# Kernel tuning notes

Hardware: AMD Instinct MI355X
Metric: run time of the kernel (lower is better)

The kernel has to match this reference:

```python
import jax, jax.numpy as jnp
import numpy as np
from jax import lax

SHIFT = 32  # shift_range from init
EPS_NORM = 1e-12
EPS_MASK = 1e-6


def _l2_normalize_flat(x):
    # F.normalize(x.reshape(B,-1)): per-sample L2 normalize with eps 1e-12
    B = x.shape[0]
    flat = x.reshape(B, -1)
    n = jnp.linalg.norm(flat, axis=1, keepdims=True)
    return (flat / jnp.maximum(n, EPS_NORM)).reshape(x.shape)


def setup_inputs() -> dict:
    key = jax.random.key(0)
    k1, k2 = jax.random.split(key)
    grd_feature = jax.random.normal(k1, (8, 32, 32, 32), dtype=jnp.float32)
    sat_feature = jax.random.normal(k2, (8, 32, 128, 128), dtype=jnp.float32)
    return {"grd_feature": grd_feature, "sat_feature": sat_feature, "test_method": 1}


def reference(grd_feature, sat_feature, test_method):
    # test_method == 1 path (default); test_method in {0,1} only differ in divisor
    M, C, H_s, W_s = sat_feature.shape
    N, _, H, W = grd_feature.shape
    kH = min(H, H_s - 2 * SHIFT)
    kW = min(W, W_s - 2 * SHIFT)

    # center-crop ground template to (kH, kW) and L2-normalize per sample
    gh0, gw0 = H // 2 - kH // 2, W // 2 - kW // 2
    grd = grd_feature[:, :, gh0:gh0 + 2 * (kH // 2), gw0:gw0 + 2 * (kW // 2)]
    N_, _, H_k, W_k = grd.shape
    grd = _l2_normalize_flat(grd)

    # center-crop satellite to search region and L2-normalize per sample
    sh0 = H_s // 2 - SHIFT - kH // 2
    sw0 = W_s // 2 - SHIFT - kW // 2
    sat = sat_feature[:, :, sh0:sh0 + 2 * (SHIFT + kH // 2), sw0:sw0 + 2 * (SHIFT + kW // 2)]
    _, _, H_i, W_i = sat.shape
    sat = _l2_normalize_flat(sat)

    # all-pairs cross-correlation: corr[m, n, y, x] (torch grouped-conv on repeated sat
    # is equivalent to a plain VALID conv of sat with all N ground filters)
    corr = lax.conv_general_dilated(
        sat, grd, window_strides=(1, 1), padding='VALID',
        dimension_numbers=('NCHW', 'OIHW', 'NCHW'))  # [M, N, Ho, Wo]
    Ho, Wo = corr.shape[2], corr.shape[3]

    # sliding-window sum of |sat|^2 (avg_pool with divisor_override=1, summed over C)
    s2 = jnp.sum(sat * sat, axis=1)  # [M, H_i, W_i]
    partical = lax.reduce_window(s2, jnp.float32(0), lax.add,
                                 (1, H_k, W_k), (1, 1, 1), 'VALID')  # [M, Ho, Wo]
    if test_method == 0:
        denom = jnp.sqrt(partical)
    else:
        denom = partical
    corr = corr / jnp.maximum(denom[:, None], EPS_NORM)

    similarity_matrix = jnp.max(corr, axis=(2, 3))  # [M, N]

    # diagonal pairs (m == n): peak localization
    diag = jnp.diagonal(corr, axis1=0, axis2=1)        # [Ho, Wo, M]
    diag = jnp.transpose(diag, (2, 0, 1)).reshape(M, -1)
    max_index = jnp.argmax(diag, axis=-1)
    pos_h = max_index // Wo
    pos_w = max_index % Wo

    grd_mask = (jnp.abs(jnp.sum(grd, axis=1)) > EPS_MASK).astype(jnp.float32)  # [N, H_k, W_k]

    def place(ph, pw, gm):
        z = jnp.zeros((1, H_i, W_i), dtype=jnp.float32)
        return lax.dynamic_update_slice(z, gm[None], (0, ph, pw))

    mask = jax.vmap(place)(pos_h, pos_w, grd_mask)  # [M, 1, H_i, W_i]
    return similarity_matrix, mask
```

## Files before the change

kernel.cpp:

```cpp
#include <hip/hip_runtime.h>
#include <stdint.h>

typedef unsigned short u16;
typedef unsigned int u32;
typedef unsigned long long u64;
typedef __bf16 bf16x8 __attribute__((ext_vector_type(8)));
typedef float floatx4 __attribute__((ext_vector_type(4)));

#define DEVI static __device__ __forceinline__

DEVI u16 f2bf(float f) {
  uint32_t u = __builtin_bit_cast(uint32_t, f);
  u += 0x7FFFu + ((u >> 16) & 1u);
  return (u16)(u >> 16);
}
DEVI float bf2f(u16 b) { return __builtin_bit_cast(float, (uint32_t)b << 16); }

DEVI u32 encf(float f) {
  u32 u = __builtin_bit_cast(u32, f);
  return (u >> 31) ? ~u : (u | 0x80000000u);
}
DEVI float decf(u32 e) {
  u32 u = (e >> 31) ? (e & 0x7FFFFFFFu) : ~e;
  return __builtin_bit_cast(float, u);
}

static constexpr size_t OFF_CORRP = 0;
static constexpr size_t OFF_SATT  = OFF_CORRP + (size_t)4*270400*4;
static constexpr size_t OFF_GRDP  = OFF_SATT + (size_t)8*4*96*96*8*2;
static constexpr size_t OFF_S2    = OFF_GRDP + (size_t)4*1024*16*8*2;
static constexpr size_t OFF_PART  = OFF_S2   + (size_t)73728*4;
static constexpr size_t OFF_NRMP  = OFF_PART + (size_t)33800*4;
static constexpr size_t OFF_GNRM  = OFF_NRMP + 768*4;
static constexpr size_t OFF_MASK  = OFF_GNRM + 32;
static constexpr size_t OFF_PMAX  = OFF_MASK + (size_t)8192*4;
static constexpr size_t OFF_CNT   = OFF_PMAX + 320*4;
static constexpr size_t OFF_CAND  = OFF_CNT  + 512;

__global__ __launch_bounds__(256) void k_prep(
    const float* __restrict__ grd, const float* __restrict__ sat,
    u16* __restrict__ sTh, u16* __restrict__ gP,
    float* __restrict__ s2, float* __restrict__ nrmp,
    float* __restrict__ gnrm, float* __restrict__ gmask,
    u32* __restrict__ cnts) {
  __shared__ float L[32*100];
  __shared__ float red[256];
  const int t = threadIdx.x;
  if (blockIdx.x < 768) {
    const int m = blockIdx.x / 96, y = blockIdx.x - (blockIdx.x / 96) * 96;
    #pragma unroll
    for (int k = 0; k < 3; ++k) {
      const int idx = k*256 + t;
      const int c = idx / 24, xq = idx - c*24;
      const float4 v = *(const float4*)(sat + (((size_t)m*32 + c)*128 + (16+y))*128 + 16 + xq*4);
      *(float4*)(&L[c*100 + xq*4]) = v;
    }
    __syncthreads();
    float ss = 0.f;
    if (t < 96) {
      #pragma unroll
      for (int c = 0; c < 32; ++c) { const float v = L[c*100 + t]; ss += v*v; }
      s2[(size_t)m*9216 + y*96 + t] = ss;
    }
    red[t] = ss; __syncthreads();
    for (int s = 128; s > 0; s >>= 1) { if (t < s) red[t] += red[t+s]; __syncthreads(); }
    if (t == 0) nrmp[m*96 + y] = red[0];
    for (int idx = t; idx < 384; idx += 256) {
      const int cb = idx / 96, x = idx - cb*96;
      union { u16 us[8]; uint4 v4; } P;
      #pragma unroll
      for (int e = 0; e < 8; ++e) P.us[e] = f2bf(L[(cb*8+e)*100 + x]);
      *(uint4*)(&sTh[(((size_t)m*4+cb)*9216 + (size_t)y*96 + x)*8]) = P.v4;
    }
  } else if (blockIdx.x == 776) {
    if (t < 72) cnts[t] = 0u;
  } else {
    const int n = blockIdx.x - 768;
    float nn = 0.f, scs[4];
    #pragma unroll
    for (int it = 0; it < 4; ++it) {
      const int pidx = it*256 + t;
      float vals[32]; float sc = 0.f;
      #pragma unroll
      for (int c = 0; c < 32; ++c) {
        const float v = grd[((size_t)n*32 + c)*1024 + pidx];
        vals[c] = v; sc += v; nn += v*v;
      }
      scs[it] = sc;
      #pragma unroll
      for (int cb = 0; cb < 4; ++cb) {
        union { u16 us[8]; uint4 v4; } ph, pl;
        #pragma unroll
        for (int e = 0; e < 8; ++e) {
          const float v = vals[cb*8+e];
          const u16 h = f2bf(v); ph.us[e] = h; pl.us[e] = f2bf(v - bf2f(h));
        }
        const size_t o = ((size_t)cb*1024 + pidx)*128;
        *(uint4*)(&gP[o + (size_t)n*8])     = ph.v4;
        *(uint4*)(&gP[o + (size_t)(n+8)*8]) = pl.v4;
      }
    }
    red[t] = nn; __syncthreads();
    for (int s = 128; s > 0; s >>= 1) { if (t < s) red[t] += red[t+s]; __syncthreads(); }
    const float gn = fmaxf(sqrtf(red[0]), 1e-12f);
    if (t == 0) gnrm[n] = red[0];
    const float thr = 1e-6f * gn;
    #pragma unroll
    for (int it = 0; it < 4; ++it)
      gmask[n*1024 + it*256 + t] = (fabsf(scs[it]) > thr) ? 1.f : 0.f;
  }
}

__global__ __launch_bounds__(256, 4) void k_conv(
    const u16* __restrict__ satT, const u16* __restrict__ gP,
    const float* __restrict__ s2, float* __restrict__ corr_p,
    float* __restrict__ part)
{
  __shared__ __align__(16) u16 patch[36*48*8];

  const int bi = blockIdx.x;
  const int tid = threadIdx.x;

  if (bi >= 1824) {
    float* S  = (float*)patch;
    float* HS = S + 40*96;
    const int pb = bi - 1824;
    const int pm = pb / 9, ysl = (pb - pm*9)*8;
    const int nrows = (65 - ysl) < 8 ? (65 - ysl) : 8;
    const int scnt  = (96 - ysl) < 40 ? (96 - ysl) : 40;
    for (int idx = tid; idx < scnt*96; idx += 256)
      S[idx] = s2[(size_t)pm*9216 + (size_t)ysl*96 + idx];
    __syncthreads();
    const int hrows = nrows + 31;
    for (int idx = tid; idx < hrows*65; idx += 256) {
      const int r = idx / 65, xo = idx - r*65;
      const float* p = &S[r*96 + xo];
      float s = 0.f;
      #pragma unroll
      for (int j = 0; j < 32; ++j) s += p[j];
      HS[idx] = s;
    }
    __syncthreads();
    for (int idx = tid; idx < nrows*65; idx += 256) {
      const int r = idx / 65, xo = idx - r*65;
      float s = 0.f;
      #pragma unroll
      for (int i = 0; i < 32; ++i) s += HS[(r+i)*65 + xo];
      part[(size_t)pm*4225 + (size_t)(ysl+r)*65 + xo] = s;
    }
    return;
  }

  const int wave = tid >> 6, lane = tid & 63;
  const int pr = lane & 15, q = lane >> 4;

  if (bi >= 1664) {
    const int e = bi - 1664;
    const int cb = e & 3;
    const int yt = (e >> 2) % 5;
    const int m  = e / 20;
    const int ybase = yt * 13;
    const size_t rowbase = ((size_t)(m*4 + cb) * 96 + ybase) * 96;
    for (int k = tid; k < 44*32; k += 256) {
      const int rho = k >> 5, px = k & 31;
      *(uint4*)(&patch[(size_t)k*8]) =
          *(const uint4*)(&satT[(rowbase + (size_t)rho*96 + 64 + px)*8]);
    }
    __syncthreads();
    const int prc = pr < 13 ? pr : 12;
    floatx4 acc = (floatx4){0.f, 0.f, 0.f, 0.f};
    #pragma unroll
    for (int jbi = 0; jbi < 2; ++jbi) {
      const int jb = wave*2 + jbi;
      const int px_e = jb*4 + q;
      const u16* bp = gP + ((size_t)cb*1024 + (size_t)(jb*4+q))*128 + (size_t)pr*8;
      uint4 Br[8];
      #pragma unroll
      for (int ii = 0; ii < 8; ++ii) Br[ii] = *(const uint4*)(bp + (size_t)ii*4096);
      uint4 Ah[8];
      #pragma unroll
      for (int s = 0; s < 6; ++s)
        Ah[s] = *(const uint4*)(&patch[((size_t)(prc + s)*32 + px_e)*8]);
      #pragma unroll
      for (int i = 0; i < 32; ++i) {
        if (i < 26)
          Ah[(i+6)&7] = *(const uint4*)(&patch[((size_t)(prc + i + 6)*32 + px_e)*8]);
        const bf16x8 bf = __builtin_bit_cast(bf16x8, Br[i&7]);
        if (i < 24)
          Br[(i+8)&7] = *(const uint4*)(bp + (size_t)(i+8)*4096);
        acc = __builtin_amdgcn_mfma_f32_16x16x32_bf16(
            __builtin_bit_cast(bf16x8, Ah[i&7]), bf, acc, 0, 0, 0);
      }
    }
    float v4[4];
    #pragma unroll
    for (int k = 0; k < 4; ++k) v4[k] = acc[k] + __shfl_xor(acc[k], 8);
    __syncthreads();
    float* red = (float*)patch;
    #pragma unroll
    for (int k = 0; k < 4; ++k) red[((size_t)wave*64 + lane)*5 + k] = v4[k];
    __syncthreads();
    if (wave == 0 && pr < 8) {
      #pragma unroll
      for (int k = 0; k < 4; ++k) {
        const int yoff = q*4 + k;
        if (yoff < 13) {
          float s = 0.f;
          #pragma unroll
          for (int w = 0; w < 4; ++w) s += red[((size_t)w*64 + lane)*5 + k];
          corr_p[(size_t)cb*270400 + ((size_t)(m*8+pr)*65 + (ybase+yoff))*65 + 64] = s;
        }
      }
    }
    return;
  }

  int b = bi;
  const int cb = b & 3; b >>= 2;
  const int xt = b % 4; b /= 4;
  const int yt = b % 13;
  const int m  = b / 13;
  const int y0 = yt*5, x0 = xt*16;

  {
    const size_t rowbase = ((size_t)(m*4 + cb) * 96 + y0) * 96;
    for (int k = tid; k < 36*48; k += 256) {
      const int rho = k / 48;
      const int px  = k - rho*48;
      *(uint4*)(&patch[(size_t)k*8]) =
          *(const uint4*)(&satT[(rowbase + (size_t)rho*96 + x0 + px)*8]);
    }
  }
  __syncthreads();

  floatx4 acc[5];
  #pragma unroll
  for (int r = 0; r < 5; ++r) acc[r] = (floatx4){0.f, 0.f, 0.f, 0.f};

  #pragma unroll
  for (int jbi = 0; jbi < 2; ++jbi) {
    const int jb = wave*2 + jbi;
    const int apx = pr + jb*4 + q;
    const u16* bp = gP + ((size_t)cb*1024 + (size_t)(jb*4+q))*128 + (size_t)pr*8;

    uint4 Br[8];
    #pragma unroll
    for (int ii = 0; ii < 8; ++ii) Br[ii] = *(const uint4*)(bp + (size_t)ii*4096);
    uint4 Ah[8];
    #pragma unroll
    for (int s = 0; s < 6; ++s) Ah[s] = *(const uint4*)(&patch[((size_t)s*48 + apx)*8]);

    #pragma unroll
    for (int i = 0; i < 32; ++i) {
      if (i < 30)
        Ah[(i+6)&7] = *(const uint4*)(&patch[((size_t)(i+6)*48 + apx)*8]);
      const bf16x8 bf = __builtin_bit_cast(bf16x8, Br[i&7]);
      if (i < 24)
        Br[(i+8)&7] = *(const uint4*)(bp + (size_t)(i+8)*4096);
      #pragma unroll
      for (int r = 0; r < 5; ++r)
        acc[r] = __builtin_amdgcn_mfma_f32_16x16x32_bf16(
            __builtin_bit_cast(bf16x8, Ah[(i+r)&7]), bf, acc[r], 0, 0, 0);
    }
  }

  float vals[20];
  #pragma unroll
  for (int r = 0; r < 5; ++r)
    #pragma unroll
    for (int k = 0; k < 4; ++k)
      vals[r*4+k] = acc[r][k] + __shfl_xor(acc[r][k], 8);

  __syncthreads();
  float* red = (float*)patch;
  #pragma unroll
  for (int u = 0; u < 20; ++u) red[((size_t)wave*64 + lane)*21 + u] = vals[u];
  __syncthreads();
  if (wave == 0 && pr < 8) {
    #pragma unroll
    for (int r = 0; r < 5; ++r) {
      #pragma unroll
      for (int k = 0; k < 4; ++k) {
        const int x = x0 + q*4 + k;
        float s = 0.f;
        #pragma unroll
        for (int w = 0; w < 4; ++w) s += red[((size_t)w*64 + lane)*21 + r*4 + k];
        corr_p[(size_t)cb*270400 + ((size_t)(m*8+pr)*65 + (y0+r))*65 + x] = s;
      }
    }
  }
}

__global__ __launch_bounds__(256) void k_post(
    const float* __restrict__ corr_p, const float* __restrict__ part,
    const float* __restrict__ nrmp, const float* __restrict__ gnrm,
    const int* __restrict__ tm, const float* __restrict__ grd,
    const float* __restrict__ sat, const float* __restrict__ gmask,
    u32* __restrict__ pmaxE, u32* __restrict__ grpcnt,
    u32* __restrict__ candcnt, u64* __restrict__ cand,
    float* __restrict__ out)
{
  __shared__ float red[256];
  __shared__ float s_bcast;
  __shared__ int s_last;
  __shared__ int fidx[128];
  __shared__ u32 fcnt;

  const int bi = blockIdx.x;
  const int m = bi / 40, n = (bi / 5) & 7, yc = bi % 5, g = m*8 + n;
  const int t = threadIdx.x;
  const bool diag = (m == n);

  red[t] = (t < 96) ? nrmp[m*96 + t] : 0.f;
  __syncthreads();
  for (int s = 128; s > 0; s >>= 1) { if (t < s) red[t] += red[t+s]; __syncthreads(); }
  const float srn = 1.f / fmaxf(sqrtf(red[0]), 1e-12f);
  const float grn = 1.f / fmaxf(sqrtf(gnrm[n]), 1e-12f);
  const float cscale = grn * srn, pscale = srn * srn;
  const int method = tm[0];

  const float* cp = corr_p + (size_t)g*4225;
  const float* pp = part + (size_t)m*4225;
  const int i0 = yc*845, i1 = i0 + 845;
  float vv[4];
  float bestv = -3.4e38f;
  #pragma unroll
  for (int k = 0; k < 4; ++k) {
    const int idx = i0 + k*256 + t;
    float v = -3.4e38f;
    if (idx < i1) {
      const float c = cp[idx] + cp[idx+270400] + cp[idx+540800] + cp[idx+811200];
      const float pt = pp[idx] * pscale;
      float denom = (method == 0) ? sqrtf(pt) : pt;
      denom = fmaxf(denom, 1e-12f);
      v = c * cscale / denom;
    }
    vv[k] = v;
    bestv = fmaxf(bestv, v);
  }
  __syncthreads();
  red[t] = bestv; __syncthreads();
  for (int s = 128; s > 0; s >>= 1) { if (t < s) red[t] = fmaxf(red[t], red[t+s]); __syncthreads(); }
  if (t == 0) { s_bcast = red[0]; atomicExch(&pmaxE[bi], encf(red[0])); }
  __syncthreads();
  if (diag) {
    const float lthr = s_bcast - 3e-3f;
    #pragma unroll
    for (int k = 0; k < 4; ++k) {
      const int idx = i0 + k*256 + t;
      if (idx < i1 && vv[k] >= lthr) {
        const u32 s = atomicAdd(&candcnt[n], 1u);
        if (s < 128)
          atomicExch(&cand[n*128 + s],
                     ((u64)__builtin_bit_cast(u32, vv[k]) << 32) | (u32)idx);
      }
    }
  }
  __syncthreads();
  if (t == 0) s_last = (atomicAdd(&grpcnt[g], 1u) == 4u) ? 1 : 0;
  __syncthreads();
  if (!s_last) return;

  if (t == 0) {
    float gm = -3.4e38f;
    #pragma unroll
    for (int k = 0; k < 5; ++k) gm = fmaxf(gm, decf(atomicOr(&pmaxE[g*5 + k], 0u)));
    out[g] = gm;
    s_bcast = gm;
  }
  __syncthreads();
  if (!diag) return;

  const float gmax = s_bcast;
  const float thr = gmax - 3e-3f;
  if (t == 0) fcnt = 0u;
  __syncthreads();
  u32 nc = atomicAdd(&candcnt[n], 0u); if (nc > 128) nc = 128;
  if (t < (int)nc) {
    const u64 pk = atomicAdd(&cand[n*128 + t], 0ULL);
    const float vf = __builtin_bit_cast(float, (u32)(pk >> 32));
    const int idx = (int)(u32)pk;
    if (vf >= thr) { const u32 s = atomicAdd(&fcnt, 1u); fidx[s] = idx; }
  }
  __syncthreads();
  if (t == 0 && fcnt == 0u) { fidx[0] = 0; fcnt = 1u; }
  __syncthreads();
  const int nf = (int)fcnt;

  __shared__ float sbest; __shared__ int sbix;
  if (t == 0) { sbest = -3.4e38f; sbix = 0x7FFFFFFF; }
  __syncthreads();
  const int c = t >> 3, s8 = t & 7;
  for (int ci = 0; ci < nf; ++ci) {
    const int idx = fidx[ci];
    const int y = idx / 65, x = idx - y*65;
    float a = 0.f;
    #pragma unroll
    for (int ii = 0; ii < 4; ++ii) {
      const int i = s8 + ii*8;
      const float* gr = grd + ((size_t)n*32 + c)*1024 + i*32;
      const float* sr = sat + (((size_t)n*32 + c)*128 + (16 + y + i))*128 + (16 + x);
      #pragma unroll
      for (int j = 0; j < 32; ++j) a += gr[j] * sr[j];
    }
    red[t] = a; __syncthreads();
    for (int st = 128; st > 0; st >>= 1) { if (t < st) red[t] += red[t+st]; __syncthreads(); }
    if (t == 0) {
      const float pt = part[(size_t)n*4225 + idx] * pscale;
      float denom = (method == 0) ? sqrtf(pt) : pt;
      denom = fmaxf(denom, 1e-12f);
      const float v = red[0] * cscale / denom;
      if (v > sbest || (v == sbest && idx < sbix)) { sbest = v; sbix = idx; }
    }
    __syncthreads();
  }
  const int bix = sbix;
  const int ph = bix / 65, pw = bix - (bix/65)*65;
  for (int p = t; p < 9216; p += 256) {
    const int yy = p / 96, xx = p - yy*96;
    float val = 0.f;
    if (yy >= ph && yy < ph+32 && xx >= pw && xx < pw+32)
      val = gmask[n*1024 + (yy-ph)*32 + (xx-pw)];
    out[64 + (size_t)n*9216 + p] = val;
  }
}

extern "C" void kernel_launch(void* const* d_in, const int* in_sizes, int n_in,
                              void* d_out, int out_size, void* d_ws, size_t ws_size,
                              hipStream_t stream) {
  const float* grd = (const float*)d_in[0];
  const float* sat = (const float*)d_in[1];
  const int*   tm  = (const int*)d_in[2];
  float* out = (float*)d_out;
  char* ws = (char*)d_ws;

  float* corrp = (float*)(ws + OFF_CORRP);
  u16*   sTh   = (u16*)(ws + OFF_SATT);
  u16*   gP    = (u16*)(ws + OFF_GRDP);
  float* s2    = (float*)(ws + OFF_S2);
  float* part  = (float*)(ws + OFF_PART);
  float* nrmp  = (float*)(ws + OFF_NRMP);
  float* gnrm  = (float*)(ws + OFF_GNRM);
  float* gmask = (float*)(ws + OFF_MASK);
  u32*   pmaxE = (u32*)(ws + OFF_PMAX);
  u32*   cnts  = (u32*)(ws + OFF_CNT);
  u64*   cand  = (u64*)(ws + OFF_CAND);

  k_prep<<<777,  256, 0, stream>>>(grd, sat, sTh, gP, s2, nrmp, gnrm, gmask, cnts);
  k_conv<<<1896, 256, 0, stream>>>(sTh, gP, s2, corrp, part);
  k_post<<<320,  256, 0, stream>>>(corrp, part, nrmp, gnrm, tm, grd, sat, gmask,
                                   pmaxE, cnts, cnts + 64, cand, out);
}
```

Baseline: 148.9 us.

## Enlarge conv output tile to ten rows and stage patches via global_load_lds

The main conv blocks now compute 10 output rows instead of 5, so each block reuses each loaded ground-filter B fragment across twice as many MFMAs. This halves B-operand global traffic and cuts the block count, with a 5-row remainder tile for the last rows. Satellite patch staging switches to direct global-to-LDS loads, which skips the trip through registers. In exchange, register pressure rises (10 accumulators, 12 A registers), so launch bounds drop to 3 blocks per CU, and the LDS patch grows.

```diff
diff --git a/kernel.cpp b/kernel.cpp
--- a/kernel.cpp
+++ b/kernel.cpp
@@ -23,6 +23,16 @@
 DEVI float decf(u32 e) {
   u32 u = (e >> 31) ? (e & 0x7FFFFFFFu) : ~e;
   return __builtin_bit_cast(float, u);
+}
+
+DEVI void cp16(const u16* g, u16* l) {
+#if __has_builtin(__builtin_amdgcn_global_load_lds)
+  __builtin_amdgcn_global_load_lds(
+      (const __attribute__((address_space(1))) uint32_t*)g,
+      (__attribute__((address_space(3))) uint32_t*)l, 16, 0, 0);
+#else
+  *(uint4*)l = *(const uint4*)g;
+#endif
 }
 
 static constexpr size_t OFF_CORRP = 0;
@@ -111,20 +121,20 @@
   }
 }
 
-__global__ __launch_bounds__(256, 4) void k_conv(
+__global__ __launch_bounds__(256, 3) void k_conv(
     const u16* __restrict__ satT, const u16* __restrict__ gP,
     const float* __restrict__ s2, float* __restrict__ corr_p,
     float* __restrict__ part)
 {
-  __shared__ __align__(16) u16 patch[36*48*8];
+  __shared__ __align__(16) u16 patch[41*48*8];
 
   const int bi = blockIdx.x;
   const int tid = threadIdx.x;
 
-  if (bi >= 1824) {
+  if (bi >= 1056) {
     float* S  = (float*)patch;
     float* HS = S + 40*96;
-    const int pb = bi - 1824;
+    const int pb = bi - 1056;
     const int pm = pb / 9, ysl = (pb - pm*9)*8;
     const int nrows = (65 - ysl) < 8 ? (65 - ysl) : 8;
     const int scnt  = (96 - ysl) < 40 ? (96 - ysl) : 40;
@@ -154,8 +164,8 @@
   const int wave = tid >> 6, lane = tid & 63;
   const int pr = lane & 15, q = lane >> 4;
 
-  if (bi >= 1664) {
-    const int e = bi - 1664;
+  if (bi >= 896) {
+    const int e = bi - 896;
     const int cb = e & 3;
     const int yt = (e >> 2) % 5;
     const int m  = e / 20;
@@ -163,9 +173,9 @@
     const size_t rowbase = ((size_t)(m*4 + cb) * 96 + ybase) * 96;
     for (int k = tid; k < 44*32; k += 256) {
       const int rho = k >> 5, px = k & 31;
-      *(uint4*)(&patch[(size_t)k*8]) =
-          *(const uint4*)(&satT[(rowbase + (size_t)rho*96 + 64 + px)*8]);
-    }
+      cp16(&satT[(rowbase + (size_t)rho*96 + 64 + px)*8], &patch[(size_t)k*8]);
+    }
+    asm volatile("s_waitcnt vmcnt(0)" ::: "memory");
     __syncthreads();
     const int prc = pr < 13 ? pr : 12;
     floatx4 acc = (floatx4){0.f, 0.f, 0.f, 0.f};
@@ -217,75 +227,144 @@
 
   int b = bi;
   const int cb = b & 3; b >>= 2;
-  const int xt = b % 4; b /= 4;
-  const int yt = b % 13;
-  const int m  = b / 13;
-  const int y0 = yt*5, x0 = xt*16;
-
-  {
+  const int xt = b & 3; b >>= 2;
+  const int yt = b % 7;
+  const int m  = b / 7;
+  const int x0 = xt*16;
+
+  if (yt < 6) {
+    const int y0 = yt*10;
+    const size_t rowbase = ((size_t)(m*4 + cb) * 96 + y0) * 96;
+    for (int k = tid; k < 41*48; k += 256) {
+      const int rho = k / 48, px = k - (k/48)*48;
+      cp16(&satT[(rowbase + (size_t)rho*96 + x0 + px)*8], &patch[(size_t)k*8]);
+    }
+    asm volatile("s_waitcnt vmcnt(0)" ::: "memory");
+    __syncthreads();
+
+    floatx4 acc[10];
+    #pragma unroll
+    for (int r = 0; r < 10; ++r) acc[r] = (floatx4){0.f, 0.f, 0.f, 0.f};
+
+    #pragma unroll
+    for (int jbi = 0; jbi < 2; ++jbi) {
+      const int jb = wave*2 + jbi;
+      const int apx = pr + jb*4 + q;
+      const u16* bp = gP + ((size_t)cb*1024 + (size_t)(jb*4+q))*128 + (size_t)pr*8;
+
+      uint4 Br[8];
+      #pragma unroll
+      for (int ii = 0; ii < 8; ++ii) Br[ii] = *(const uint4*)(bp + (size_t)ii*4096);
+      uint4 Ah[12];
+      #pragma unroll
+      for (int s = 0; s < 12; ++s) Ah[s] = *(const uint4*)(&patch[((size_t)s*48 + apx)*8]);
+
+      #pragma unroll
+      for (int i = 0; i < 32; ++i) {
+        const bf16x8 bf = __builtin_bit_cast(bf16x8, Br[i&7]);
+        if (i < 24)
+          Br[(i+8)&7] = *(const uint4*)(bp + (size_t)(i+8)*4096);
+        #pragma unroll
+        for (int r = 0; r < 10; ++r)
+          acc[r] = __builtin_amdgcn_mfma_f32_16x16x32_bf16(
+              __builtin_bit_cast(bf16x8, Ah[(i+r)%12]), bf, acc[r], 0, 0, 0);
+        if (i < 29)
+          Ah[(i+12)%12] = *(const uint4*)(&patch[((size_t)(i+12)*48 + apx)*8]);
+      }
+    }
+
+    float vals[40];
+    #pragma unroll
+    for (int r = 0; r < 10; ++r)
+      #pragma unroll
+      for (int k = 0; k < 4; ++k)
+        vals[r*4+k] = acc[r][k] + __shfl_xor(acc[r][k], 8);
+
+    float* red = (float*)patch;
+    #pragma unroll
+    for (int half = 0; half < 2; ++half) {
+      __syncthreads();
+      #pragma unroll
+      for (int u = 0; u < 20; ++u) red[((size_t)wave*64 + lane)*21 + u] = vals[half*20 + u];
+      __syncthreads();
+      if (wave == 0 && pr < 8) {
+        #pragma unroll
+        for (int r = 0; r < 5; ++r) {
+          #pragma unroll
+          for (int k = 0; k < 4; ++k) {
+            const int x = x0 + q*4 + k;
+            float s = 0.f;
+            #pragma unroll
+            for (int w = 0; w < 4; ++w) s += red[((size_t)w*64 + lane)*21 + r*4 + k];
+            corr_p[(size_t)cb*270400 + ((size_t)(m*8+pr)*65 + (y0 + half*5 + r))*65 + x] = s;
+          }
+        }
+      }
+    }
+  } else {
+    const int y0 = 60;
     const size_t rowbase = ((size_t)(m*4 + cb) * 96 + y0) * 96;
     for (int k = tid; k < 36*48; k += 256) {
-      const int rho = k / 48;
-      const int px  = k - rho*48;
-      *(uint4*)(&patch[(size_t)k*8]) =
-          *(const uint4*)(&satT[(rowbase + (size_t)rho*96 + x0 + px)*8]);
-    }
-  }
-  __syncthreads();
-
-  floatx4 acc[5];
-  #pragma unroll
-  for (int r = 0; r < 5; ++r) acc[r] = (floatx4){0.f, 0.f, 0.f, 0.f};
-
-  #pragma unroll
-  for (int jbi = 0; jbi < 2; ++jbi) {
-    const int jb = wave*2 + jbi;
-    const int apx = pr + jb*4 + q;
-    const u16* bp = gP + ((size_t)cb*1024 + (size_t)(jb*4+q))*128 + (size_t)pr*8;
-
-    uint4 Br[8];
-    #pragma unroll
-    for (int ii = 0; ii < 8; ++ii) Br[ii] = *(const uint4*)(bp + (size_t)ii*4096);
-    uint4 Ah[8];
-    #pragma unroll
-    for (int s = 0; s < 6; ++s) Ah[s] = *(const uint4*)(&patch[((size_t)s*48 + apx)*8]);
-
-    #pragma unroll
-    for (int i = 0; i < 32; ++i) {
-      if (i < 30)
-        Ah[(i+6)&7] = *(const uint4*)(&patch[((size_t)(i+6)*48 + apx)*8]);
-      const bf16x8 bf = __builtin_bit_cast(bf16x8, Br[i&7]);
-      if (i < 24)
-        Br[(i+8)&7] = *(const uint4*)(bp + (size_t)(i+8)*4096);
-      #pragma unroll
-      for (int r = 0; r < 5; ++r)
-        acc[r] = __builtin_amdgcn_mfma_f32_16x16x32_bf16(
-            __builtin_bit_cast(bf16x8, Ah[(i+r)&7]), bf, acc[r], 0, 0, 0);
-    }
-  }
-
-  float vals[20];
-  #pragma unroll
-  for (int r = 0; r < 5; ++r)
-    #pragma unroll
-    for (int k = 0; k < 4; ++k)
-      vals[r*4+k] = acc[r][k] + __shfl_xor(acc[r][k], 8);
-
-  __syncthreads();
-  float* red = (float*)patch;
-  #pragma unroll
-  for (int u = 0; u < 20; ++u) red[((size_t)wave*64 + lane)*21 + u] = vals[u];
-  __syncthreads();
-  if (wave == 0 && pr < 8) {
-    #pragma unroll
-    for (int r = 0; r < 5; ++r) {
-      #pragma unroll
-      for (int k = 0; k < 4; ++k) {
-        const int x = x0 + q*4 + k;
-        float s = 0.f;
+      const int rho = k / 48, px = k - (k/48)*48;
+      cp16(&satT[(rowbase + (size_t)rho*96 + x0 + px)*8], &patch[(size_t)k*8]);
+    }
+    asm volatile("s_waitcnt vmcnt(0)" ::: "memory");
+    __syncthreads();
+
+    floatx4 acc[5];
+    #pragma unroll
+    for (int r = 0; r < 5; ++r) acc[r] = (floatx4){0.f, 0.f, 0.f, 0.f};
+
+    #pragma unroll
+    for (int jbi = 0; jbi < 2; ++jbi) {
+      const int jb = wave*2 + jbi;
+      const int apx = pr + jb*4 + q;
+      const u16* bp = gP + ((size_t)cb*1024 + (size_t)(jb*4+q))*128 + (size_t)pr*8;
+
+      uint4 Br[8];
+      #pragma unroll
+      for (int ii = 0; ii < 8; ++ii) Br[ii] = *(const uint4*)(bp + (size_t)ii*4096);
+      uint4 Ah[8];
+      #pragma unroll
+      for (int s = 0; s < 6; ++s) Ah[s] = *(const uint4*)(&patch[((size_t)s*48 + apx)*8]);
+
+      #pragma unroll
+      for (int i = 0; i < 32; ++i) {
+        if (i < 30)
+          Ah[(i+6)&7] = *(const uint4*)(&patch[((size_t)(i+6)*48 + apx)*8]);
+        const bf16x8 bf = __builtin_bit_cast(bf16x8, Br[i&7]);
+        if (i < 24)
+          Br[(i+8)&7] = *(const uint4*)(bp + (size_t)(i+8)*4096);
         #pragma unroll
-        for (int w = 0; w < 4; ++w) s += red[((size_t)w*64 + lane)*21 + r*4 + k];
-        corr_p[(size_t)cb*270400 + ((size_t)(m*8+pr)*65 + (y0+r))*65 + x] = s;
+        for (int r = 0; r < 5; ++r)
+          acc[r] = __builtin_amdgcn_mfma_f32_16x16x32_bf16(
+              __builtin_bit_cast(bf16x8, Ah[(i+r)&7]), bf, acc[r], 0, 0, 0);
+      }
+    }
+
+    float vals[20];
+    #pragma unroll
+    for (int r = 0; r < 5; ++r)
+      #pragma unroll
+      for (int k = 0; k < 4; ++k)
+        vals[r*4+k] = acc[r][k] + __shfl_xor(acc[r][k], 8);
+
+    __syncthreads();
+    float* red = (float*)patch;
+    #pragma unroll
+    for (int u = 0; u < 20; ++u) red[((size_t)wave*64 + lane)*21 + u] = vals[u];
+    __syncthreads();
+    if (wave == 0 && pr < 8) {
+      #pragma unroll
+      for (int r = 0; r < 5; ++r) {
+        #pragma unroll
+        for (int k = 0; k < 4; ++k) {
+          const int x = x0 + q*4 + k;
+          float s = 0.f;
+          #pragma unroll
+          for (int w = 0; w < 4; ++w) s += red[((size_t)w*64 + lane)*21 + r*4 + k];
+          corr_p[(size_t)cb*270400 + ((size_t)(m*8+pr)*65 + (y0+r))*65 + x] = s;
+        }
       }
     }
   }
@@ -447,7 +526,7 @@
   u64*   cand  = (u64*)(ws + OFF_CAND);
 
   k_prep<<<777,  256, 0, stream>>>(grd, sat, sTh, gP, s2, nrmp, gnrm, gmask, cnts);
-  k_conv<<<1896, 256, 0, stream>>>(sTh, gP, s2, corrp, part);
+  k_conv<<<1128, 256, 0, stream>>>(sTh, gP, s2, corrp, part);
   k_post<<<320,  256, 0, stream>>>(corrp, part, nrmp, gnrm, tm, grd, sat, gmask,
                                    pmaxE, cnts, cnts + 64, cand, out);
 }
```

Measured after the change: 147.6 us. Within noise of the previous version (-0.9%).
